# Kernel tuning notes

Hardware: AMD Instinct MI355X
Metric: run time of the kernel (lower is better)

## Reference

```python
import jax, jax.numpy as jnp
import numpy as np

E, H = 1024, 16
D = E // H


def softmax_1(x):
    # softmax_1: exp(x_i) / (1 + sum_j exp(x_j)), computed stably
    m = jnp.max(x, axis=-1, keepdims=True)
    e = jnp.exp(x - m)
    return e / (jnp.exp(-m) + jnp.sum(e, axis=-1, keepdims=True))


def setup_inputs() -> dict:
    key = jax.random.key(0)
    ks = jax.random.split(key, 8)
    S, B = 1024, 4
    x = jax.random.normal(ks[0], (S, B, E), dtype=jnp.float32)
    attn_bias = jax.random.normal(ks[1], (B, H, S, S), dtype=jnp.float32)
    attn_bias_mul = jax.random.uniform(ks[2], (B, H, S, S), dtype=jnp.float32)
    key_padding_mask = jax.random.randint(ks[3], (B, S), 0, 2).astype(jnp.bool_)
    # xavier-ish init for linear layers (torch Linear: y = x @ W.T + b)
    W_in = jax.random.normal(ks[4], (3 * E, E), dtype=jnp.float32) * (E ** -0.5)
    b_in = jnp.zeros((3 * E,), dtype=jnp.float32)
    W_out = jax.random.normal(ks[5], (E, E), dtype=jnp.float32) * (E ** -0.5)
    b_out = jnp.zeros((E,), dtype=jnp.float32)
    return {"x": x, "attn_bias": attn_bias, "attn_bias_mul": attn_bias_mul,
            "key_padding_mask": key_padding_mask,
            "W_in": W_in, "b_in": b_in, "W_out": W_out, "b_out": b_out}


def reference(x, attn_bias, attn_bias_mul, key_padding_mask, W_in, b_in, W_out, b_out):
    S, B, _ = x.shape
    # in_proj -> [S, B, 3E] -> [B*H, S, 3D]
    qkv = x @ W_in.T + b_in
    qkv = qkv.reshape(S, B * H, 3 * D).transpose(1, 0, 2)
    q, k, v = jnp.split(qkv, 3, axis=-1)
    q = q * (D ** -0.5)
    # scores [B*H, S, S] with additive bias
    aw = jnp.einsum('bqd,bkd->bqk', q, k) + attn_bias.reshape(B * H, S, S)
    # key padding mask (dropout p=0 -> identity)
    kpm = key_padding_mask[:, None, None, :]  # [B,1,1,S]
    aw = jnp.where(kpm, -jnp.inf, aw.reshape(B, H, S, S)).reshape(B * H, S, S)
    abm = jnp.where(kpm, 0.0, attn_bias_mul).reshape(B * H, S, S)
    p = softmax_1(aw) * abm
    attn = jnp.einsum('bqk,bkd->bqd', p, v)  # [B*H, S, D]
    attn = attn.transpose(1, 0, 2).reshape(S, B, E)
    return attn @ W_out.T + b_out
```

## Files before the change

kernel.cpp:

```cpp
#include <hip/hip_runtime.h>
#include <stdint.h>
#include <stddef.h>

typedef __attribute__((ext_vector_type(4))) float f32x4;
typedef __attribute__((ext_vector_type(4))) int   i32x4;
typedef __attribute__((ext_vector_type(8))) short s16x8;
typedef __attribute__((ext_vector_type(4))) short s16x4;
typedef __attribute__((ext_vector_type(8))) __bf16 bf16x8;

#define AS3 __attribute__((address_space(3)))
#define AS1 __attribute__((address_space(1)))

__device__ inline void gload16(const void* g, void* l) {
  __builtin_amdgcn_global_load_lds((AS1 const void*)g, (AS3 void*)l, 16, 0, 0);
}

__device__ inline f32x4 mfma16(s16x8 a, s16x8 b, f32x4 c) {
  return __builtin_amdgcn_mfma_f32_16x16x32_bf16(
      __builtin_bit_cast(bf16x8, a), __builtin_bit_cast(bf16x8, b), c, 0, 0, 0);
}

__device__ inline short f2bf(float f) {
  unsigned u = __builtin_bit_cast(unsigned, f);
  u += 0x7FFFu + ((u >> 16) & 1u);
  return (short)(u >> 16);
}
__device__ inline float bf2f(short x) {
  unsigned u = ((unsigned)(unsigned short)x) << 16;
  return __builtin_bit_cast(float, u);
}

__global__ void cast_all(const float* __restrict__ x, const float* __restrict__ wi,
                         const float* __restrict__ wo, short* __restrict__ xb,
                         short* __restrict__ wib, short* __restrict__ wob) {
  int i = blockIdx.x * 256 + threadIdx.x;
  const float* src;
  short* dst;
  int off;
  if (i < 1048576)      { src = x;  dst = xb;  off = i; }
  else if (i < 1835008) { src = wi; dst = wib; off = i - 1048576; }
  else                  { src = wo; dst = wob; off = i - 1835008; }
  f32x4 v = *(const f32x4*)(src + (size_t)off * 4);
  s16x4 o;
#pragma unroll
  for (int r = 0; r < 4; ++r) o[r] = f2bf(v[r]);
  *(s16x4*)(dst + (size_t)off * 4) = o;
}

template <int OBF, int FR>
__global__ __launch_bounds__(256, 2) void gemm_bt(
    const short* __restrict__ A, const short* __restrict__ B,
    const float* __restrict__ bias, void* __restrict__ Cv,
    int M, int N, int K) {
  const int TILE = FR * 32;
  const int tid = threadIdx.x, w = tid >> 6, lane = tid & 63;
  const int quad = lane >> 4, l15 = lane & 15;
  const int wm = w >> 1, wn = w & 1;
  const int m0 = blockIdx.y * TILE, n0 = blockIdx.x * TILE;
  __shared__ short As[TILE * 32], Bs[TILE * 32];
  f32x4 acc[FR][FR];
#pragma unroll
  for (int i = 0; i < FR; ++i)
#pragma unroll
    for (int j = 0; j < FR; ++j) acc[i][j] = (f32x4){0.f, 0.f, 0.f, 0.f};
  const int rs = lane >> 2, cs = (lane & 3) * 8;
  const int nkt = K >> 5;
  for (int kt = 0; kt < nkt; ++kt) {
    const int k0 = kt * 32;
#pragma unroll
    for (int j = 0; j < FR / 2; ++j) {
      gload16(A + (size_t)(m0 + w * (FR * 8) + j * 16 + rs) * K + k0 + cs,
              &As[w * (FR * 256) + j * 512]);
      gload16(B + (size_t)(n0 + w * (FR * 8) + j * 16 + rs) * K + k0 + cs,
              &Bs[w * (FR * 256) + j * 512]);
    }
    __syncthreads();
    s16x8 af[FR], bfr[FR];
#pragma unroll
    for (int i = 0; i < FR; ++i) {
      af[i]  = *(const s16x8*)&As[(wm * (FR * 16) + i * 16 + l15) * 32 + quad * 8];
      bfr[i] = *(const s16x8*)&Bs[(wn * (FR * 16) + i * 16 + l15) * 32 + quad * 8];
    }
#pragma unroll
    for (int ms = 0; ms < FR; ++ms)
#pragma unroll
      for (int ns = 0; ns < FR; ++ns)
        acc[ms][ns] = mfma16(af[ms], bfr[ns], acc[ms][ns]);
    __syncthreads();
  }
#pragma unroll
  for (int ms = 0; ms < FR; ++ms) {
    const int row0 = m0 + wm * (FR * 16) + ms * 16 + quad * 4;
#pragma unroll
    for (int ns = 0; ns < FR; ++ns) {
      const int col = n0 + wn * (FR * 16) + ns * 16 + l15;
      const float bv = bias[col];
#pragma unroll
      for (int r = 0; r < 4; ++r) {
        float v = acc[ms][ns][r] + bv;
        if (OBF) ((short*)Cv)[(size_t)(row0 + r) * N + col] = f2bf(v);
        else     ((float*)Cv)[(size_t)(row0 + r) * N + col] = v;
      }
    }
  }
}

__global__ void repack_all(const short* __restrict__ qkv, short* __restrict__ qh,
                           short* __restrict__ kh, short* __restrict__ vT) {
  __shared__ short t[64][80];
  const int bh = blockIdx.x, st_ = blockIdx.y;
  const int b_ = bh >> 4, h_ = bh & 15;
  const int tid = threadIdx.x;
#pragma unroll
  for (int part = 0; part < 4; ++part) {
    int lin = part * 256 + tid;
    int dg = lin & 7, ty = (lin >> 3) & 1, s_l = lin >> 4;
    int s = st_ * 64 + s_l;
    s16x8 v = *(const s16x8*)(qkv + (size_t)(s * 4 + b_) * 3072 + h_ * 192 + ty * 64 + dg * 8);
    if (ty == 0) {
#pragma unroll
      for (int i = 0; i < 8; ++i) v[i] = f2bf(bf2f(v[i]) * 0.125f);
      *(s16x8*)&qh[((size_t)bh << 16) + (size_t)s * 64 + dg * 8] = v;
    } else {
      *(s16x8*)&kh[((size_t)bh << 16) + (size_t)s * 64 + dg * 8] = v;
    }
  }
#pragma unroll
  for (int part = 0; part < 2; ++part) {
    int lin = part * 256 + tid;
    int ch = lin & 7, s_l = lin >> 3;
    int s = st_ * 64 + s_l;
    *(s16x8*)&t[s_l][ch * 8] =
        *(const s16x8*)(qkv + (size_t)(s * 4 + b_) * 3072 + h_ * 192 + 128 + ch * 8);
  }
  __syncthreads();
#pragma unroll
  for (int part = 0; part < 2; ++part) {
    int lin = part * 256 + tid;
    int sc = lin & 7, d_l = lin >> 3;
    s16x8 vv;
#pragma unroll
    for (int j = 0; j < 8; ++j) vv[j] = t[sc * 8 + j][d_l];
    *(s16x8*)&vT[((size_t)bh << 16) + (size_t)d_l * 1024 + st_ * 64 + sc * 8] = vv;
  }
}

__global__ __launch_bounds__(256, 4) void attn_fused(
    const short* __restrict__ qh, const short* __restrict__ kh,
    const short* __restrict__ vT, const float* __restrict__ bias,
    const float* __restrict__ abm, const int* __restrict__ kpm,
    short* __restrict__ attnbf) {
  const int tid = threadIdx.x;
  const int w = tid >> 6, lane = tid & 63, quad = lane >> 4, l15 = lane & 15;
  const int bh = blockIdx.x, qb = blockIdx.y;
  const int b_ = bh >> 4, h_ = bh & 15;
  const short* qhd = qh + ((size_t)bh << 16);
  const short* khd = kh + ((size_t)bh << 16);
  const short* vTd = vT + ((size_t)bh << 16);
  const float* biasd = bias + ((size_t)bh << 20);
  const float* abmd  = abm  + ((size_t)bh << 20);
  const int*   kpmd  = kpm + (b_ << 10);
  const int qw = qb * 64 + w * 16;

  __shared__ short kbuf[2][32 * 64];
  __shared__ short vbuf[2][64 * 32];
  __shared__ short wl[4][16 * 40];
  __shared__ float alds[4][16];

  s16x8 qf[2];
#pragma unroll
  for (int t = 0; t < 2; ++t)
    qf[t] = *(const s16x8*)&qhd[(size_t)(qw + l15) * 64 + t * 32 + quad * 8];

  f32x4 o[4];
#pragma unroll
  for (int ds = 0; ds < 4; ++ds) o[ds] = (f32x4){0.f, 0.f, 0.f, 0.f};
  float mrun = -1e30f, lrun = 0.f;

  struct Pack { f32x4 bs[2]; f32x4 ab[2]; i32x4 kp[2]; };
  Pack P0, P1;

  auto stage = [&](int kt, int pb) {
    gload16(khd + (size_t)kt * 2048 + w * 512 + lane * 8, &kbuf[pb][w * 512]);
    gload16(vTd + (size_t)(w * 16 + (lane >> 2)) * 1024 + kt * 32 + (lane & 3) * 8,
            &vbuf[pb][w * 512]);
  };
  auto loadP = [&](int kt, Pack& P) {
    const int kb = kt * 32;
    const size_t qrow = (size_t)(qw + l15) * 1024;
#pragma unroll
    for (int ms = 0; ms < 2; ++ms) {
      P.bs[ms] = *(const f32x4*)&biasd[qrow + kb + ms * 16 + quad * 4];
      P.ab[ms] = *(const f32x4*)&abmd [qrow + kb + ms * 16 + quad * 4];
      P.kp[ms] = *(const i32x4*)&kpmd[kb + ms * 16 + quad * 4];
    }
  };

  auto compute = [&](int pb, Pack& P) {
    const f32x4 z4 = {0.f, 0.f, 0.f, 0.f};
    f32x4 st[2];
#pragma unroll
    for (int ms = 0; ms < 2; ++ms) {
      s16x8 a0 = *(const s16x8*)&kbuf[pb][(ms * 16 + l15) * 64 + quad * 8];
      s16x8 a1 = *(const s16x8*)&kbuf[pb][(ms * 16 + l15) * 64 + 32 + quad * 8];
      st[ms] = mfma16(a1, qf[1], mfma16(a0, qf[0], z4));
    }
    float mloc = -1e30f;
#pragma unroll
    for (int ms = 0; ms < 2; ++ms)
#pragma unroll
      for (int r = 0; r < 4; ++r) {
        float sc = st[ms][r] + P.bs[ms][r];
        sc = (P.kp[ms][r] != 0) ? -1e30f : sc;
        st[ms][r] = sc;
        mloc = fmaxf(mloc, sc);
      }
    mloc = fmaxf(mloc, __shfl_xor(mloc, 16));
    mloc = fmaxf(mloc, __shfl_xor(mloc, 32));
    float mn = fmaxf(mrun, mloc);
    float al = __expf(mrun - mn);
    mrun = mn;
    float lloc = 0.f;
#pragma unroll
    for (int ms = 0; ms < 2; ++ms)
#pragma unroll
      for (int r = 0; r < 4; ++r) {
        float e = (P.kp[ms][r] != 0) ? 0.f : __expf(st[ms][r] - mrun);
        st[ms][r] = e;
        lloc += e;
      }
    lloc += __shfl_xor(lloc, 16);
    lloc += __shfl_xor(lloc, 32);
    lrun = lrun * al + lloc;
    alds[w][l15] = al;
#pragma unroll
    for (int ms = 0; ms < 2; ++ms) {
      s16x4 pk;
#pragma unroll
      for (int r = 0; r < 4; ++r) pk[r] = f2bf(st[ms][r] * P.ab[ms][r]);
      *(s16x4*)&wl[w][l15 * 40 + ms * 16 + quad * 4] = pk;
    }
    f32x4 av = *(const f32x4*)&alds[w][quad * 4];
    s16x8 pf = *(const s16x8*)&wl[w][l15 * 40 + quad * 8];
#pragma unroll
    for (int ds = 0; ds < 4; ++ds) o[ds] *= av;
#pragma unroll
    for (int ds = 0; ds < 4; ++ds) {
      s16x8 vf = *(const s16x8*)&vbuf[pb][(ds * 16 + l15) * 32 + quad * 8];
      o[ds] = mfma16(pf, vf, o[ds]);
    }
  };

  stage(0, 0);
  loadP(0, P0);
  __syncthreads();
  for (int kt = 0; kt < 32; kt += 2) {
    stage(kt + 1, 1);
    loadP(kt + 1, P1);
    compute(0, P0);
    __syncthreads();
    if (kt + 2 < 32) { stage(kt + 2, 0); loadP(kt + 2, P0); }
    compute(1, P1);
    __syncthreads();
  }

  float rd = 1.f / (__expf(-mrun) + lrun);
  alds[w][l15] = rd;
  f32x4 rdv = *(const f32x4*)&alds[w][quad * 4];
#pragma unroll
  for (int ds = 0; ds < 4; ++ds) {
    f32x4 ov = o[ds] * rdv;
#pragma unroll
    for (int r = 0; r < 4; ++r) {
      int s = qw + quad * 4 + r;
      attnbf[(size_t)(s * 4 + b_) * 1024 + h_ * 64 + ds * 16 + l15] = f2bf(ov[r]);
    }
  }
}

extern "C" void kernel_launch(void* const* d_in, const int* in_sizes, int n_in,
                              void* d_out, int out_size, void* d_ws, size_t ws_size,
                              hipStream_t stream) {
  const float* x     = (const float*)d_in[0];
  const float* bias  = (const float*)d_in[1];
  const float* abm   = (const float*)d_in[2];
  const int*   kpm   = (const int*)  d_in[3];
  const float* W_in  = (const float*)d_in[4];
  const float* b_in  = (const float*)d_in[5];
  const float* W_out = (const float*)d_in[6];
  const float* b_out = (const float*)d_in[7];
  float* out = (float*)d_out;

  char* ws = (char*)d_ws;
  short* xbf    = (short*)(ws);
  short* wibf   = (short*)(ws + (8u << 20));
  short* wobf   = (short*)(ws + (14u << 20) + (512u << 10));
  short* qkvbf  = (short*)(ws + (16u << 20) + (768u << 10));
  short* qh     = (short*)(ws + (40u << 20) + (768u << 10));
  short* kh     = (short*)(ws + (48u << 20) + (768u << 10));
  short* vTh    = (short*)(ws + (56u << 20) + (768u << 10));
  short* attnbf = (short*)(ws + (64u << 20) + (768u << 10));

  cast_all<<<8192, 256, 0, stream>>>(x, W_in, W_out, xbf, wibf, wobf);

  gemm_bt<1, 4><<<dim3(24, 32), 256, 0, stream>>>(xbf, wibf, b_in, (void*)qkvbf,
                                                  4096, 3072, 1024);

  repack_all<<<dim3(64, 16), 256, 0, stream>>>(qkvbf, qh, kh, vTh);

  attn_fused<<<dim3(64, 16), 256, 0, stream>>>(qh, kh, vTh, bias, abm, kpm, attnbf);

  gemm_bt<0, 2><<<dim3(16, 64), 256, 0, stream>>>(attnbf, wobf, b_out, (void*)out,
                                                  4096, 1024, 1024);
}
```

Measured before the change: 646.2 us.

## Read K and V fragments directly from global memory, dropping LDS staging and barriers

The attention kernel no longer stages K and V tiles into shared memory with async global-to-LDS loads. Each wave now reads its MFMA fragments for K and V^T straight from global memory, relying on L1/L2 for the reuse across the four waves. Block-wide __syncthreads are removed, and the bias/mask prefetch is rescheduled two tiles ahead. This trades LDS traffic and barrier stalls for redundant global/cache loads, plus K/V load latency that now sits directly in front of the MFMAs.

```diff
diff --git a/kernel.cpp b/kernel.cpp
--- a/kernel.cpp
+++ b/kernel.cpp
@@ -154,23 +154,20 @@
   const int w = tid >> 6, lane = tid & 63, quad = lane >> 4, l15 = lane & 15;
   const int bh = blockIdx.x, qb = blockIdx.y;
   const int b_ = bh >> 4, h_ = bh & 15;
-  const short* qhd = qh + ((size_t)bh << 16);
   const short* khd = kh + ((size_t)bh << 16);
   const short* vTd = vT + ((size_t)bh << 16);
-  const float* biasd = bias + ((size_t)bh << 20);
-  const float* abmd  = abm  + ((size_t)bh << 20);
+  const int qw = qb * 64 + w * 16;
+  const float* biasd = bias + ((size_t)bh << 20) + (size_t)(qw + l15) * 1024;
+  const float* abmd  = abm  + ((size_t)bh << 20) + (size_t)(qw + l15) * 1024;
   const int*   kpmd  = kpm + (b_ << 10);
-  const int qw = qb * 64 + w * 16;
-
-  __shared__ short kbuf[2][32 * 64];
-  __shared__ short vbuf[2][64 * 32];
+
   __shared__ short wl[4][16 * 40];
   __shared__ float alds[4][16];
 
   s16x8 qf[2];
 #pragma unroll
   for (int t = 0; t < 2; ++t)
-    qf[t] = *(const s16x8*)&qhd[(size_t)(qw + l15) * 64 + t * 32 + quad * 8];
+    qf[t] = *(const s16x8*)&qh[((size_t)bh << 16) + (size_t)(qw + l15) * 64 + t * 32 + quad * 8];
 
   f32x4 o[4];
 #pragma unroll
@@ -180,29 +177,28 @@
   struct Pack { f32x4 bs[2]; f32x4 ab[2]; i32x4 kp[2]; };
   Pack P0, P1;
 
-  auto stage = [&](int kt, int pb) {
-    gload16(khd + (size_t)kt * 2048 + w * 512 + lane * 8, &kbuf[pb][w * 512]);
-    gload16(vTd + (size_t)(w * 16 + (lane >> 2)) * 1024 + kt * 32 + (lane & 3) * 8,
-            &vbuf[pb][w * 512]);
-  };
   auto loadP = [&](int kt, Pack& P) {
     const int kb = kt * 32;
-    const size_t qrow = (size_t)(qw + l15) * 1024;
 #pragma unroll
     for (int ms = 0; ms < 2; ++ms) {
-      P.bs[ms] = *(const f32x4*)&biasd[qrow + kb + ms * 16 + quad * 4];
-      P.ab[ms] = *(const f32x4*)&abmd [qrow + kb + ms * 16 + quad * 4];
+      P.bs[ms] = *(const f32x4*)&biasd[kb + ms * 16 + quad * 4];
+      P.ab[ms] = *(const f32x4*)&abmd [kb + ms * 16 + quad * 4];
       P.kp[ms] = *(const i32x4*)&kpmd[kb + ms * 16 + quad * 4];
     }
   };
 
-  auto compute = [&](int pb, Pack& P) {
+  auto compute = [&](int kt, Pack& P) {
+    const int kb = kt * 32;
     const f32x4 z4 = {0.f, 0.f, 0.f, 0.f};
+    s16x8 vf[4];
+#pragma unroll
+    for (int ds = 0; ds < 4; ++ds)
+      vf[ds] = *(const s16x8*)&vTd[(size_t)(ds * 16 + l15) * 1024 + kb + quad * 8];
     f32x4 st[2];
 #pragma unroll
     for (int ms = 0; ms < 2; ++ms) {
-      s16x8 a0 = *(const s16x8*)&kbuf[pb][(ms * 16 + l15) * 64 + quad * 8];
-      s16x8 a1 = *(const s16x8*)&kbuf[pb][(ms * 16 + l15) * 64 + 32 + quad * 8];
+      s16x8 a0 = *(const s16x8*)&khd[(size_t)(kb + ms * 16 + l15) * 64 + quad * 8];
+      s16x8 a1 = *(const s16x8*)&khd[(size_t)(kb + ms * 16 + l15) * 64 + 32 + quad * 8];
       st[ms] = mfma16(a1, qf[1], mfma16(a0, qf[0], z4));
     }
     float mloc = -1e30f;
@@ -245,23 +241,17 @@
 #pragma unroll
     for (int ds = 0; ds < 4; ++ds) o[ds] *= av;
 #pragma unroll
-    for (int ds = 0; ds < 4; ++ds) {
-      s16x8 vf = *(const s16x8*)&vbuf[pb][(ds * 16 + l15) * 32 + quad * 8];
-      o[ds] = mfma16(pf, vf, o[ds]);
-    }
+    for (int ds = 0; ds < 4; ++ds)
+      o[ds] = mfma16(pf, vf[ds], o[ds]);
   };
 
-  stage(0, 0);
   loadP(0, P0);
-  __syncthreads();
+  loadP(1, P1);
   for (int kt = 0; kt < 32; kt += 2) {
-    stage(kt + 1, 1);
-    loadP(kt + 1, P1);
-    compute(0, P0);
-    __syncthreads();
-    if (kt + 2 < 32) { stage(kt + 2, 0); loadP(kt + 2, P0); }
-    compute(1, P1);
-    __syncthreads();
+    compute(kt, P0);
+    if (kt + 2 < 32) loadP(kt + 2, P0);
+    compute(kt + 1, P1);
+    if (kt + 3 < 32) loadP(kt + 3, P1);
   }
 
   float rd = 1.f / (__expf(-mrun) + lrun);
```

Result: slower. 705.7 us (+9.2%).
